# Performance work log

Measured on AMD Instinct MI355X. Metric: run time of the kernel, lower is better.

Reference implementation:

```python
import jax, jax.numpy as jnp
import numpy as np

EMB = 1024
HEADS = 16
DH = EMB // HEADS
EPS = 1e-5


def setup_inputs() -> dict:
    key = jax.random.key(0)
    ks = jax.random.split(key, 8)
    s = 0.02
    return {
        "x": jax.random.normal(ks[0], (4, 2048, EMB), dtype=jnp.float32),
        "Wq": jax.random.normal(ks[1], (EMB, EMB), dtype=jnp.float32) * s,
        "Wk": jax.random.normal(ks[2], (EMB, EMB), dtype=jnp.float32) * s,
        "Wv": jax.random.normal(ks[3], (EMB, EMB), dtype=jnp.float32) * s,
        "Wo": jax.random.normal(ks[4], (EMB, EMB), dtype=jnp.float32) * s,
        "bo": jnp.zeros((EMB,), dtype=jnp.float32),
        "W1": jax.random.normal(ks[5], (EMB, 4 * EMB), dtype=jnp.float32) * s,
        "b1": jnp.zeros((4 * EMB,), dtype=jnp.float32),
        "W2": jax.random.normal(ks[6], (4 * EMB, EMB), dtype=jnp.float32) * s,
        "b2": jnp.zeros((EMB,), dtype=jnp.float32),
        "g1": jnp.ones((EMB,), dtype=jnp.float32),
        "beta1": jnp.zeros((EMB,), dtype=jnp.float32),
        "g2": jnp.ones((EMB,), dtype=jnp.float32),
        "beta2": jnp.zeros((EMB,), dtype=jnp.float32),
    }


def _layernorm(x, scale, bias):
    mean = jnp.mean(x, axis=-1, keepdims=True)
    var = jnp.mean((x - mean) ** 2, axis=-1, keepdims=True)  # unbiased=False
    return scale * ((x - mean) / jnp.sqrt(var + EPS)) + bias


def _attention(x, Wq, Wk, Wv, Wo, bo):
    B, S, _ = x.shape
    q = (x @ Wq).reshape(B, S, HEADS, DH).transpose(0, 2, 1, 3)  # b h s d
    k = (x @ Wk).reshape(B, S, HEADS, DH).transpose(0, 2, 1, 3)
    v = (x @ Wv).reshape(B, S, HEADS, DH).transpose(0, 2, 1, 3)
    scores = jnp.einsum("bhqd,bhkd->bhqk", q, k)
    causal = jnp.tril(jnp.ones((S, S), dtype=bool))
    scores = jnp.where(causal, scores, -jnp.inf)
    w = jax.nn.softmax(scores / jnp.sqrt(jnp.float32(DH)), axis=-1)
    ctx = jnp.einsum("bhqk,bhkd->bhqd", w, v).transpose(0, 2, 1, 3).reshape(B, S, HEADS * DH)
    return ctx @ Wo + bo


def reference(x, Wq, Wk, Wv, Wo, bo, W1, b1, W2, b2, g1, beta1, g2, beta2):
    # pre-LN attention + residual
    h = x + _attention(_layernorm(x, g1, beta1), Wq, Wk, Wv, Wo, bo)
    # pre-LN FFN (exact GELU, as torch nn.GELU default) + residual
    y = _layernorm(h, g2, beta2)
    y = jax.nn.gelu(y @ W1 + b1, approximate=False) @ W2 + b2
    return h + y
```

## Files before the change

kernel.cpp:

```cpp
#include <hip/hip_runtime.h>
#include <hip/hip_bf16.h>

#define EMB 1024
#define SEQ 2048
#define BATCH 4
#define TOK (BATCH*SEQ)
#define NH 16
#define DH 64
#define FF 4096

typedef unsigned short u16;
typedef __bf16 bf16x8 __attribute__((ext_vector_type(8)));
typedef float f32x4 __attribute__((ext_vector_type(4)));

union frag_u { uint4 u4; bf16x8 bf; u16 us[8]; };

__device__ __forceinline__ u16 f2bf(float f) {
  union { float f; unsigned u; } a; a.f = f;
  unsigned r = a.u + 0x7fffu + ((a.u >> 16) & 1u);
  return (u16)(r >> 16);
}
__device__ __forceinline__ float bf2f(u16 u) {
  union { unsigned u; float f; } a; a.u = ((unsigned)u) << 16; return a.f;
}

__device__ __forceinline__ void glds16(const void* g, void* l) {
  __builtin_amdgcn_global_load_lds((const __attribute__((address_space(1))) void*)g,
                                   (__attribute__((address_space(3))) void*)l, 16, 0, 0);
}

__device__ __forceinline__ float gelu_fast(float u) {
  float u2 = u * u;
  float c = fmaf(u2, 0.0356774081f, 0.7978845608f);
  float e = __expf(2.f * u * c);
  return u * e * __builtin_amdgcn_rcpf(e + 1.f);
}

__device__ __forceinline__ void cvt_t_body(const float* __restrict__ src,
                                           u16* __restrict__ dst,
                                           int N, int ldk, int bx, int by) {
  __shared__ float tile[32][33];
  int c0 = bx * 32, r0 = by * 32;
  int tc = threadIdx.x & 31, tr = threadIdx.x >> 5;
  #pragma unroll
  for (int p = 0; p < 4; p++)
    tile[tr + p * 8][tc] = src[(size_t)(r0 + tr + p * 8) * N + c0 + tc];
  __syncthreads();
  #pragma unroll
  for (int p = 0; p < 4; p++)
    dst[(size_t)(c0 + tr + p * 8) * ldk + r0 + tc] = f2bf(tile[tc][tr + p * 8]);
}

__global__ __launch_bounds__(256) void prep_kernel(const float* Wq, const float* Wk,
                                                   const float* Wv, const float* Wo,
                                                   const float* W1, const float* W2,
                                                   u16* wqkv_t, u16* wo_t,
                                                   u16* w1_t, u16* w2_t) {
  int id = blockIdx.x;
  if (id < 4096) {
    const float* s = (id < 1024) ? Wq : (id < 2048) ? Wk : (id < 3072) ? Wv : Wo;
    u16* d = (id < 1024) ? wqkv_t : (id < 2048) ? wqkv_t + 1024 * 1024
           : (id < 3072) ? wqkv_t + 2 * 1024 * 1024 : wo_t;
    int local = id & 1023;
    cvt_t_body(s, d, 1024, 1024, local & 31, local >> 5);
  } else if (id < 8192) {
    int local = id - 4096;
    cvt_t_body(W1, w1_t, 4096, 1024, local & 127, local >> 7);
  } else {
    int local = id - 8192;
    cvt_t_body(W2, w2_t, 1024, 4096, local & 31, local >> 5);
  }
}

template <int IN_BF16>
__global__ __launch_bounds__(256) void ln_kernel(const void* __restrict__ xv,
                                                 const float* __restrict__ g,
                                                 const float* __restrict__ be,
                                                 u16* __restrict__ out) {
  int wave = threadIdx.x >> 6, lane = threadIdx.x & 63;
  int row = blockIdx.x * 4 + wave;
  float v[16];
  float s = 0.f;
  if (IN_BF16) {
    const u16* xr = (const u16*)xv + (size_t)row * EMB;
    #pragma unroll
    for (int i = 0; i < 4; i++) {
      ushort4 u = *(const ushort4*)(xr + i * 256 + lane * 4);
      v[i * 4 + 0] = bf2f(u.x); v[i * 4 + 1] = bf2f(u.y);
      v[i * 4 + 2] = bf2f(u.z); v[i * 4 + 3] = bf2f(u.w);
      s += v[i * 4] + v[i * 4 + 1] + v[i * 4 + 2] + v[i * 4 + 3];
    }
  } else {
    const float* xr = (const float*)xv + (size_t)row * EMB;
    #pragma unroll
    for (int i = 0; i < 4; i++) {
      float4 u = *(const float4*)(xr + i * 256 + lane * 4);
      v[i * 4 + 0] = u.x; v[i * 4 + 1] = u.y; v[i * 4 + 2] = u.z; v[i * 4 + 3] = u.w;
      s += u.x + u.y + u.z + u.w;
    }
  }
  #pragma unroll
  for (int m = 1; m < 64; m <<= 1) s += __shfl_xor(s, m, 64);
  float mean = s * (1.f / EMB);
  float vs = 0.f;
  #pragma unroll
  for (int i = 0; i < 16; i++) { float dx = v[i] - mean; vs += dx * dx; }
  #pragma unroll
  for (int m = 1; m < 64; m <<= 1) vs += __shfl_xor(vs, m, 64);
  float inv = rsqrtf(vs * (1.f / EMB) + 1e-5f);
  u16* orow = out + (size_t)row * EMB;
  #pragma unroll
  for (int i = 0; i < 4; i++) {
    int c = i * 256 + lane * 4;
    float4 gv = *(const float4*)(g + c);
    float4 bv = *(const float4*)(be + c);
    ushort4 o;
    o.x = f2bf(gv.x * (v[i * 4 + 0] - mean) * inv + bv.x);
    o.y = f2bf(gv.y * (v[i * 4 + 1] - mean) * inv + bv.y);
    o.z = f2bf(gv.z * (v[i * 4 + 2] - mean) * inv + bv.z);
    o.w = f2bf(gv.w * (v[i * 4 + 3] - mean) * inv + bv.w);
    *(ushort4*)(orow + c) = o;
  }
}

template <int MODE>
__global__ __launch_bounds__(512) void gemm256(const u16* __restrict__ A,
                                               const u16* __restrict__ Bt,
                                               const float* __restrict__ bias,
                                               void* __restrict__ outp,
                                               int N, int K) {
  __shared__ __align__(16) u16 As[256 * 64];
  __shared__ __align__(16) u16 Bs[128 * 64];
  const int t = threadIdx.x;
  const int w = t >> 6, lane = t & 63;
  const int l15 = lane & 15, quad = lane >> 4;
  const int wr = w >> 1, wc = w & 1;
  const int rowBase = blockIdx.y * 256, colBase = blockIdx.x * 128;

  const int sr = lane >> 3;
  const int sc = ((lane & 7) ^ sr) * 8;
  const u16* gA = A + (size_t)(rowBase + w * 8 + sr) * K + sc;
  const u16* gB = Bt + (size_t)(colBase + w * 8 + sr) * K + sc;
  u16* lA = As + w * 8 * 64;
  u16* lB = Bs + w * 8 * 64;

  const int swz0 = (quad ^ (l15 & 7)) * 8;
  const int swz1 = ((quad + 4) ^ (l15 & 7)) * 8;

  f32x4 zero = {0.f, 0.f, 0.f, 0.f};
  f32x4 acc[4][4];
  #pragma unroll
  for (int i = 0; i < 4; i++)
    #pragma unroll
    for (int j = 0; j < 4; j++) acc[i][j] = zero;

  for (int k0 = 0; k0 < K; k0 += 64) {
    __syncthreads();
    #pragma unroll
    for (int j = 0; j < 4; j++)
      glds16(gA + (size_t)(j * 64) * K + k0, lA + j * 64 * 64);
    #pragma unroll
    for (int j = 0; j < 2; j++)
      glds16(gB + (size_t)(j * 64) * K + k0, lB + j * 64 * 64);
    __syncthreads();
    #pragma unroll
    for (int kk = 0; kk < 2; kk++) {
      const int so = kk ? swz1 : swz0;
      frag_u a4[4], b4[4];
      #pragma unroll
      for (int mi = 0; mi < 4; mi++)
        a4[mi].u4 = *(const uint4*)(As + (wr * 64 + mi * 16 + l15) * 64 + so);
      #pragma unroll
      for (int ni = 0; ni < 4; ni++)
        b4[ni].u4 = *(const uint4*)(Bs + (wc * 64 + ni * 16 + l15) * 64 + so);
      #pragma unroll
      for (int mi = 0; mi < 4; mi++)
        #pragma unroll
        for (int ni = 0; ni < 4; ni++)
          acc[mi][ni] = __builtin_amdgcn_mfma_f32_16x16x32_bf16(a4[mi].bf, b4[ni].bf, acc[mi][ni], 0, 0, 0);
    }
  }

  #pragma unroll
  for (int mi = 0; mi < 4; mi++) {
    #pragma unroll
    for (int ni = 0; ni < 4; ni++) {
      int col = colBase + wc * 64 + ni * 16 + l15;
      int row0 = rowBase + wr * 64 + mi * 16 + quad * 4;
      if (MODE == 1) {
        int mat = col >> 10, cc = col & 1023;
        int hh = cc >> 6, d = cc & 63;
        int b = row0 >> 11, s0 = row0 & 2047;
        if (mat == 2) {
          uint2 pk;
          pk.x = (unsigned)f2bf(acc[mi][ni][0]) | ((unsigned)f2bf(acc[mi][ni][1]) << 16);
          pk.y = (unsigned)f2bf(acc[mi][ni][2]) | ((unsigned)f2bf(acc[mi][ni][3]) << 16);
          *(uint2*)((u16*)outp + 2 * (size_t)TOK * EMB +
                    ((size_t)((b * NH + hh) * DH + d)) * SEQ + s0) = pk;
        } else {
          #pragma unroll
          for (int r = 0; r < 4; r++)
            ((u16*)outp)[(size_t)mat * (TOK * EMB) +
                         (((size_t)(b * NH + hh) * SEQ + s0 + r) << 6) + d] = f2bf(acc[mi][ni][r]);
        }
      } else {
        #pragma unroll
        for (int r = 0; r < 4; r++) {
          float vv = gelu_fast(acc[mi][ni][r] + bias[col]);
          ((u16*)outp)[(size_t)(row0 + r) * N + col] = f2bf(vv);
        }
      }
    }
  }
}

template <int MODE>
__global__ __launch_bounds__(256) void gemm128(const u16* __restrict__ A,
                                               const u16* __restrict__ Bt,
                                               const float* __restrict__ bias,
                                               const void* __restrict__ resid,
                                               void* __restrict__ outp,
                                               int N, int K) {
  __shared__ __align__(16) u16 As[128 * 64];
  __shared__ __align__(16) u16 Bs[128 * 64];
  const int t = threadIdx.x;
  const int w = t >> 6, lane = t & 63;
  const int l15 = lane & 15, quad = lane >> 4;
  const int wr = w >> 1, wc = w & 1;
  const int rowBase = blockIdx.y * 128, colBase = blockIdx.x * 128;

  const int sr = lane >> 3;
  const int sc = ((lane & 7) ^ sr) * 8;
  const u16* gA = A + (size_t)(rowBase + w * 8 + sr) * K + sc;
  const u16* gB = Bt + (size_t)(colBase + w * 8 + sr) * K + sc;
  u16* lA = As + w * 8 * 64;
  u16* lB = Bs + w * 8 * 64;

  const int swz0 = (quad ^ (l15 & 7)) * 8;
  const int swz1 = ((quad + 4) ^ (l15 & 7)) * 8;

  f32x4 zero = {0.f, 0.f, 0.f, 0.f};
  f32x4 acc[4][4];
  #pragma unroll
  for (int i = 0; i < 4; i++)
    #pragma unroll
    for (int j = 0; j < 4; j++) acc[i][j] = zero;

  for (int k0 = 0; k0 < K; k0 += 64) {
    __syncthreads();
    #pragma unroll
    for (int j = 0; j < 4; j++) {
      glds16(gA + (size_t)(j * 32) * K + k0, lA + j * 32 * 64);
      glds16(gB + (size_t)(j * 32) * K + k0, lB + j * 32 * 64);
    }
    __syncthreads();
    #pragma unroll
    for (int kk = 0; kk < 2; kk++) {
      const int so = kk ? swz1 : swz0;
      frag_u a4[4], b4[4];
      #pragma unroll
      for (int mi = 0; mi < 4; mi++)
        a4[mi].u4 = *(const uint4*)(As + (wr * 64 + mi * 16 + l15) * 64 + so);
      #pragma unroll
      for (int ni = 0; ni < 4; ni++)
        b4[ni].u4 = *(const uint4*)(Bs + (wc * 64 + ni * 16 + l15) * 64 + so);
      #pragma unroll
      for (int mi = 0; mi < 4; mi++)
        #pragma unroll
        for (int ni = 0; ni < 4; ni++)
          acc[mi][ni] = __builtin_amdgcn_mfma_f32_16x16x32_bf16(a4[mi].bf, b4[ni].bf, acc[mi][ni], 0, 0, 0);
    }
  }

  #pragma unroll
  for (int mi = 0; mi < 4; mi++) {
    #pragma unroll
    for (int ni = 0; ni < 4; ni++) {
      int col = colBase + wc * 64 + ni * 16 + l15;
      int row0 = rowBase + wr * 64 + mi * 16 + quad * 4;
      #pragma unroll
      for (int r = 0; r < 4; r++) {
        int row = row0 + r;
        float vv = acc[mi][ni][r] + bias[col];
        if (MODE == 3) {
          vv += ((const float*)resid)[(size_t)row * N + col];
          ((u16*)outp)[(size_t)row * N + col] = f2bf(vv);
        } else {
          vv += bf2f(((const u16*)resid)[(size_t)row * N + col]);
          ((float*)outp)[(size_t)row * N + col] = vv;
        }
      }
    }
  }
}

__global__ __launch_bounds__(256) void attn_kernel(const u16* __restrict__ q,
                                                   const u16* __restrict__ k,
                                                   const u16* __restrict__ vt,
                                                   u16* __restrict__ ctx) {
  __shared__ __align__(16) u16 Ks[64 * 72];
  __shared__ __align__(16) u16 Vs[64 * 72];
  __shared__ __align__(16) u16 Ps[128 * 72];
  __shared__ float Ls[128];
  const int t = threadIdx.x;
  const int w = t >> 6, lane = t & 63;
  const int l15 = lane & 15, quad = lane >> 4;
  const int bh = blockIdx.x, pr_ = blockIdx.y;
  const size_t base = (size_t)bh * SEQ * DH;
  const int bq = bh >> 4, hh = bh & 15;

  const int sr = t >> 2, scol = (t & 3) * 8;
  const u16* gK = k + base + (size_t)sr * DH + scol;
  const u16* gV = vt + base + (size_t)sr * SEQ + scol;
  u16* sK = Ks + sr * 72 + scol;
  u16* sV = Vs + sr * 72 + scol;

  f32x4 zero = {0.f, 0.f, 0.f, 0.f};
  uint4 rK0, rK1, rV0, rV1;
  rK0 = *(const uint4*)(gK);
  rK1 = *(const uint4*)(gK + 32);
  rV0 = *(const uint4*)(gV);
  rV1 = *(const uint4*)(gV + 32);

  for (int ti = 0; ti < 2; ti++) {
    const int qt = ti ? (15 - pr_) : pr_;
    const int qBase = qt * 128;
    const int ktEnd = 2 * qt + 1;

    frag_u qf[2][2];
    #pragma unroll
    for (int ni = 0; ni < 2; ni++)
      #pragma unroll
      for (int ks = 0; ks < 2; ks++)
        qf[ni][ks].u4 = *(const uint4*)(q + base +
            (size_t)(qBase + w * 32 + ni * 16 + l15) * DH + ks * 32 + quad * 8);

    f32x4 oacc[2][4];
    #pragma unroll
    for (int mi = 0; mi < 2; mi++)
      #pragma unroll
      for (int n0 = 0; n0 < 4; n0++) oacc[mi][n0] = zero;
    float l0 = 0.f, l1 = 0.f;

    for (int kt = 0; kt <= ktEnd; kt++) {
      __syncthreads();
      *(uint4*)sK = rK0; *(uint4*)(sK + 32) = rK1;
      *(uint4*)sV = rV0; *(uint4*)(sV + 32) = rV1;
      __syncthreads();
      int nkt = (kt < ktEnd) ? kt + 1 : (ti == 0 ? 0 : -1);
      if (nkt >= 0) {
        rK0 = *(const uint4*)(gK + (size_t)(nkt * 64) * DH);
        rK1 = *(const uint4*)(gK + (size_t)(nkt * 64) * DH + 32);
        rV0 = *(const uint4*)(gV + nkt * 64);
        rV1 = *(const uint4*)(gV + nkt * 64 + 32);
      }
      const int rel = kt - 2 * qt;
      if (rel == 1 && w < 2) continue;

      frag_u kf[4][2];
      #pragma unroll
      for (int mi = 0; mi < 4; mi++)
        #pragma unroll
        for (int ks = 0; ks < 2; ks++)
          kf[mi][ks].u4 = *(const uint4*)(Ks + (mi * 16 + l15) * 72 + ks * 32 + quad * 8);
      f32x4 st[4][2];
      #pragma unroll
      for (int mi = 0; mi < 4; mi++)
        #pragma unroll
        for (int ni = 0; ni < 2; ni++) st[mi][ni] = zero;
      #pragma unroll
      for (int ks = 0; ks < 2; ks++)
        #pragma unroll
        for (int mi = 0; mi < 4; mi++)
          #pragma unroll
          for (int ni = 0; ni < 2; ni++)
            st[mi][ni] = __builtin_amdgcn_mfma_f32_16x16x32_bf16(kf[mi][ks].bf, qf[ni][ks].bf, st[mi][ni], 0, 0, 0);

      const bool doMask = (rel == 0 && w < 2) || (rel == 1);
      #pragma unroll
      for (int ni = 0; ni < 2; ni++) {
        const int qrow = qBase + w * 32 + ni * 16 + l15;
        float sum = 0.f;
        u16* prow = Ps + (w * 32 + ni * 16 + l15) * 72;
        #pragma unroll
        for (int mi = 0; mi < 4; mi++) {
          float p[4];
          #pragma unroll
          for (int r = 0; r < 4; r++) {
            p[r] = __expf(st[mi][ni][r] * 0.125f);
            if (doMask && (kt * 64 + mi * 16 + quad * 4 + r) > qrow) p[r] = 0.f;
            sum += p[r];
          }
          uint2 pk;
          pk.x = (unsigned)f2bf(p[0]) | ((unsigned)f2bf(p[1]) << 16);
          pk.y = (unsigned)f2bf(p[2]) | ((unsigned)f2bf(p[3]) << 16);
          *(uint2*)(prow + mi * 16 + quad * 4) = pk;
        }
        sum += __shfl_xor(sum, 16, 64);
        sum += __shfl_xor(sum, 32, 64);
        if (ni == 0) l0 += sum; else l1 += sum;
      }

      frag_u pa[2][2];
      #pragma unroll
      for (int mi = 0; mi < 2; mi++)
        #pragma unroll
        for (int ks = 0; ks < 2; ks++)
          pa[mi][ks].u4 = *(const uint4*)(Ps + (w * 32 + mi * 16 + l15) * 72 + ks * 32 + quad * 8);
      #pragma unroll
      for (int ks = 0; ks < 2; ks++)
        #pragma unroll
        for (int n0 = 0; n0 < 4; n0++) {
          frag_u b;
          b.u4 = *(const uint4*)(Vs + (n0 * 16 + l15) * 72 + ks * 32 + quad * 8);
          #pragma unroll
          for (int mi = 0; mi < 2; mi++)
            oacc[mi][n0] = __builtin_amdgcn_mfma_f32_16x16x32_bf16(pa[mi][ks].bf, b.bf, oacc[mi][n0], 0, 0, 0);
        }
    }

    if (quad == 0) {
      Ls[w * 32 + l15] = l0;
      Ls[w * 32 + 16 + l15] = l1;
    }
    #pragma unroll
    for (int mi = 0; mi < 2; mi++) {
      float il[4];
      #pragma unroll
      for (int r = 0; r < 4; r++) il[r] = 1.f / Ls[w * 32 + mi * 16 + quad * 4 + r];
      #pragma unroll
      for (int n0 = 0; n0 < 4; n0++) {
        int s = qBase + w * 32 + mi * 16 + quad * 4;
        int col = hh * 64 + n0 * 16 + l15;
        #pragma unroll
        for (int r = 0; r < 4; r++)
          ctx[((size_t)(bq * SEQ + s + r)) * EMB + col] = f2bf(oacc[mi][n0][r] * il[r]);
      }
    }
  }
}

extern "C" void kernel_launch(void* const* d_in, const int* in_sizes, int n_in,
                              void* d_out, int out_size, void* d_ws, size_t ws_size,
                              hipStream_t stream) {
  const float* x  = (const float*)d_in[0];
  const float* Wq = (const float*)d_in[1];
  const float* Wk = (const float*)d_in[2];
  const float* Wv = (const float*)d_in[3];
  const float* Wo = (const float*)d_in[4];
  const float* bo = (const float*)d_in[5];
  const float* W1 = (const float*)d_in[6];
  const float* b1 = (const float*)d_in[7];
  const float* W2 = (const float*)d_in[8];
  const float* b2 = (const float*)d_in[9];
  const float* g1  = (const float*)d_in[10];
  const float* be1 = (const float*)d_in[11];
  const float* g2  = (const float*)d_in[12];
  const float* be2 = (const float*)d_in[13];
  float* out = (float*)d_out;
  char* ws = (char*)d_ws;
  const size_t MB = 1u << 20;

  u16* wqkv_t = (u16*)(ws + 0 * MB);
  u16* wo_t   = (u16*)(ws + 6 * MB);
  u16* w1_t   = (u16*)(ws + 8 * MB);
  u16* w2_t   = (u16*)(ws + 16 * MB);
  u16* hbuf   = (u16*)(ws + 24 * MB);
  u16* r1 = (u16*)(ws + 56 * MB);
  u16* qb = (u16*)(ws + 72 * MB);
  u16* f1 = (u16*)(ws + 72 * MB);

  prep_kernel<<<12288, 256, 0, stream>>>(Wq, Wk, Wv, Wo, W1, W2,
                                         wqkv_t, wo_t, w1_t, w2_t);

  ln_kernel<0><<<2048, 256, 0, stream>>>(x, g1, be1, r1);

  gemm256<1><<<dim3(24, 32), 512, 0, stream>>>(r1, wqkv_t, nullptr, qb, 3072, 1024);

  attn_kernel<<<dim3(64, 8), 256, 0, stream>>>(qb, qb + (size_t)TOK * EMB,
                                               qb + 2 * (size_t)TOK * EMB, r1);

  gemm128<3><<<dim3(8, 64), 256, 0, stream>>>(r1, wo_t, bo, x, hbuf, 1024, 1024);

  ln_kernel<1><<<2048, 256, 0, stream>>>(hbuf, g2, be2, r1);

  gemm256<2><<<dim3(32, 32), 512, 0, stream>>>(r1, w1_t, b1, f1, 4096, 1024);

  gemm128<4><<<dim3(8, 64), 256, 0, stream>>>(f1, w2_t, b2, hbuf, out, 1024, 4096);
}
```

Baseline: 498.1 us.

## Double-buffer LDS in gemm128 and remap workgroup IDs for XCD-aware L2 locality

gemm128 now keeps two LDS buffers per operand and issues the global-to-LDS loads for the next K tile before computing on the current one. This overlaps memory transfer with the MFMA work and leaves one barrier per iteration instead of two. Both GEMM kernels also remap the linear block ID so that consecutive IDs spread across the eight XCDs, grouping neighbouring tiles on the same die's L2. The double buffer doubles LDS use in gemm128, which may reduce occupancy, and the remap assumes the workgroup count is divisible by 8.

```diff
diff --git a/kernel.cpp b/kernel.cpp
--- a/kernel.cpp
+++ b/kernel.cpp
@@ -135,7 +135,12 @@
   const int w = t >> 6, lane = t & 63;
   const int l15 = lane & 15, quad = lane >> 4;
   const int wr = w >> 1, wc = w & 1;
-  const int rowBase = blockIdx.y * 256, colBase = blockIdx.x * 128;
+
+  const int gx = gridDim.x;
+  const int nwg = gx * gridDim.y;
+  const int id0 = blockIdx.y * gx + blockIdx.x;
+  const int nid = (id0 & 7) * (nwg >> 3) + (id0 >> 3);
+  const int rowBase = (nid / gx) * 256, colBase = (nid % gx) * 128;
 
   const int sr = lane >> 3;
   const int sc = ((lane & 7) ^ sr) * 8;
@@ -221,20 +226,24 @@
                                                const void* __restrict__ resid,
                                                void* __restrict__ outp,
                                                int N, int K) {
-  __shared__ __align__(16) u16 As[128 * 64];
-  __shared__ __align__(16) u16 Bs[128 * 64];
+  __shared__ __align__(16) u16 As[2][128 * 64];
+  __shared__ __align__(16) u16 Bs[2][128 * 64];
   const int t = threadIdx.x;
   const int w = t >> 6, lane = t & 63;
   const int l15 = lane & 15, quad = lane >> 4;
   const int wr = w >> 1, wc = w & 1;
-  const int rowBase = blockIdx.y * 128, colBase = blockIdx.x * 128;
+
+  const int gx = gridDim.x;
+  const int nwg = gx * gridDim.y;
+  const int id0 = blockIdx.y * gx + blockIdx.x;
+  const int nid = (id0 & 7) * (nwg >> 3) + (id0 >> 3);
+  const int rowBase = (nid / gx) * 128, colBase = (nid % gx) * 128;
 
   const int sr = lane >> 3;
   const int sc = ((lane & 7) ^ sr) * 8;
   const u16* gA = A + (size_t)(rowBase + w * 8 + sr) * K + sc;
   const u16* gB = Bt + (size_t)(colBase + w * 8 + sr) * K + sc;
-  u16* lA = As + w * 8 * 64;
-  u16* lB = Bs + w * 8 * 64;
+  const int ldsOff = (w * 8) * 64;
 
   const int swz0 = (quad ^ (l15 & 7)) * 8;
   const int swz1 = ((quad + 4) ^ (l15 & 7)) * 8;
@@ -246,30 +255,43 @@
     #pragma unroll
     for (int j = 0; j < 4; j++) acc[i][j] = zero;
 
-  for (int k0 = 0; k0 < K; k0 += 64) {
-    __syncthreads();
-    #pragma unroll
-    for (int j = 0; j < 4; j++) {
-      glds16(gA + (size_t)(j * 32) * K + k0, lA + j * 32 * 64);
-      glds16(gB + (size_t)(j * 32) * K + k0, lB + j * 32 * 64);
-    }
-    __syncthreads();
+  const int nt = K >> 6;
+  #pragma unroll
+  for (int j = 0; j < 4; j++) {
+    glds16(gA + (size_t)(j * 32) * K, As[0] + ldsOff + j * 32 * 64);
+    glds16(gB + (size_t)(j * 32) * K, Bs[0] + ldsOff + j * 32 * 64);
+  }
+  __syncthreads();
+
+  for (int tt = 0; tt < nt; tt++) {
+    const int cur = tt & 1;
+    if (tt + 1 < nt) {
+      const int k0 = (tt + 1) << 6;
+      #pragma unroll
+      for (int j = 0; j < 4; j++) {
+        glds16(gA + (size_t)(j * 32) * K + k0, As[cur ^ 1] + ldsOff + j * 32 * 64);
+        glds16(gB + (size_t)(j * 32) * K + k0, Bs[cur ^ 1] + ldsOff + j * 32 * 64);
+      }
+    }
+    const u16* as = As[cur];
+    const u16* bs = Bs[cur];
     #pragma unroll
     for (int kk = 0; kk < 2; kk++) {
       const int so = kk ? swz1 : swz0;
       frag_u a4[4], b4[4];
       #pragma unroll
       for (int mi = 0; mi < 4; mi++)
-        a4[mi].u4 = *(const uint4*)(As + (wr * 64 + mi * 16 + l15) * 64 + so);
+        a4[mi].u4 = *(const uint4*)(as + (wr * 64 + mi * 16 + l15) * 64 + so);
       #pragma unroll
       for (int ni = 0; ni < 4; ni++)
-        b4[ni].u4 = *(const uint4*)(Bs + (wc * 64 + ni * 16 + l15) * 64 + so);
+        b4[ni].u4 = *(const uint4*)(bs + (wc * 64 + ni * 16 + l15) * 64 + so);
       #pragma unroll
       for (int mi = 0; mi < 4; mi++)
         #pragma unroll
         for (int ni = 0; ni < 4; ni++)
           acc[mi][ni] = __builtin_amdgcn_mfma_f32_16x16x32_bf16(a4[mi].bf, b4[ni].bf, acc[mi][ni], 0, 0, 0);
     }
+    __syncthreads();
   }
 
   #pragma unroll
```

Measured after the change: 461.0 us. -7.4%, faster.
